# Optimization experiments

Hardware: AMD Instinct MI355X
Metric: run time of the kernel (lower is better)

The kernel has to match this reference:

```python
import jax, jax.numpy as jnp
import numpy as np

CAPACITY_FACTOR = 1.0  # fairseq Top1Gate default


def setup_inputs() -> dict:
    key = jax.random.key(0)
    ks = jax.random.split(key, 5)
    B, T, M, H, O, E = 8, 1024, 1024, 4096, 1024, 4
    return {
        "hidden_states": jax.random.normal(ks[0], (B, T, M), jnp.float32),
        "gate_w": jax.random.normal(ks[1], (M, E), jnp.float32) * 0.02,
        "fc1_w": jax.random.normal(ks[2], (E, M, H), jnp.float32) * 0.02,
        "fc1_b": jnp.zeros((E, H), jnp.float32),
        "fc2_w": jax.random.normal(ks[3], (E, H, O), jnp.float32) * 0.02,
        "fc2_b": jnp.zeros((E, O), jnp.float32),
    }


def reference(hidden_states, gate_w, fc1_w, fc1_b, fc2_w, fc2_b):
    B, T, M = hidden_states.shape
    E = gate_w.shape[1]
    S = B * T
    C = int(CAPACITY_FACTOR * -(-S // E))  # ceil(S/E)

    features = hidden_states.reshape(S, M)  # [S, M]

    # ---- Top1 gate (fairseq top1gating, eval path: no shuffle/noise) ----
    logits = features @ gate_w                      # [S, E]
    gates = jax.nn.softmax(logits, axis=1)          # [S, E]
    idx = jnp.argmax(gates, axis=1)                 # [S]
    mask1 = jax.nn.one_hot(idx, E, dtype=gates.dtype)  # [S, E]

    # load-balancing aux loss (computed before capacity dropping)
    me = jnp.mean(gates, axis=0)
    ce = jnp.mean(mask1, axis=0)
    l_aux = jnp.sum(me * ce) * E

    # capacity: position within each expert's queue; drop overflow tokens
    locations = jnp.cumsum(mask1, axis=0) - 1.0     # [S, E]
    mask1 = mask1 * (locations < C)
    loc_s = jnp.sum(locations * mask1, axis=1).astype(jnp.int32)  # [S]
    gates1_s = jnp.sum(gates * mask1, axis=1)       # [S] gate value (0 if dropped)

    # combine_weights [S, E, C] and boolean dispatch mask (as float for mm)
    combine = (gates1_s[:, None, None] * mask1[:, :, None]
               * jax.nn.one_hot(loc_s, C, dtype=gates.dtype)[:, None, :])
    dispatch = (combine > 0).astype(features.dtype)  # [S, E, C]

    # ---- dispatch via dense one-hot matmul: [E*C, S] @ [S, M] ----
    dispatch_ecs = jnp.transpose(dispatch, (1, 2, 0)).reshape(E * C, S)
    dispatched = (dispatch_ecs @ features).reshape(E, C, M)

    # ---- per-expert MLP (grouped GEMM) ----
    h = jax.nn.gelu(jnp.einsum('ecm,emh->ech', dispatched, fc1_w) + fc1_b[:, None, :])
    expert_out = jnp.einsum('ech,eho->eco', h, fc2_w) + fc2_b[:, None, :]  # [E, C, O]

    # ---- combine via dense matmul: [S, E*C] @ [E*C, O] ----
    O = expert_out.shape[-1]
    combined = combine.reshape(S, E * C) @ expert_out.reshape(E * C, O)

    return combined.reshape(B, T, O), l_aux
```

## Files before the change

kernel.cpp:

```cpp
#include <hip/hip_runtime.h>
#include <stdint.h>

#define S_TOK 8192
#define MDIM  1024
#define HDIM  4096
#define ODIM  1024
#define NEXP  4
#define CAP   2048

typedef __attribute__((ext_vector_type(8))) short short8;
typedef __attribute__((ext_vector_type(4))) float floatx4;

__device__ __forceinline__ unsigned short f2bf(float x) {
  union { float f; unsigned u; } v; v.f = x;
  unsigned r = v.u + 0x7FFFu + ((v.u >> 16) & 1u);
  return (unsigned short)(r >> 16);
}

__device__ __forceinline__ void gl_lds16(const void* g, void* l) {
  __builtin_amdgcn_global_load_lds(
      (const __attribute__((address_space(1))) void*)g,
      (__attribute__((address_space(3))) void*)l, 16, 0, 0);
}

__device__ __forceinline__ float gelu_tanh(float x) {
  float p = x * x;
  float t = x * (1.5957691216f + 0.0713548353f * p);
  float E = __expf(-t);
  return __fdividef(x, 1.0f + E);
}

__device__ __forceinline__ const char* stage_src(const char* base, int linoff,
                                                 int rowstride) {
  int row  = linoff >> 6;
  int slot = (linoff >> 4) & 3;
  int c16  = slot ^ ((row >> 1) & 3);
  return base + (size_t)row * rowstride + (c16 << 4);
}

__global__ __launch_bounds__(256) void gate_kernel(
    const float* __restrict__ feat, const float* __restrict__ gw,
    int* __restrict__ idx, float* __restrict__ gval, float* __restrict__ gsum)
{
  int wave = threadIdx.x >> 6, lane = threadIdx.x & 63;
  int s = blockIdx.x * 4 + wave;
  const float* f = feat + (size_t)s * MDIM;
  double a0 = 0, a1 = 0, a2 = 0, a3 = 0;
  #pragma unroll
  for (int j = 0; j < 16; ++j) {
    int m = lane + j * 64;
    float x = f[m];
    float4 w = ((const float4*)gw)[m];
    a0 += (double)x * w.x; a1 += (double)x * w.y;
    a2 += (double)x * w.z; a3 += (double)x * w.w;
  }
  #pragma unroll
  for (int off = 32; off; off >>= 1) {
    a0 += __shfl_down(a0, off); a1 += __shfl_down(a1, off);
    a2 += __shfl_down(a2, off); a3 += __shfl_down(a3, off);
  }
  __shared__ float bs[4];
  if (threadIdx.x < 4) bs[threadIdx.x] = 0.f;
  __syncthreads();
  if (lane == 0) {
    double lg[4] = {a0, a1, a2, a3};
    double mx = lg[0]; int bi = 0;
    #pragma unroll
    for (int e = 1; e < 4; ++e) if (lg[e] > mx) { mx = lg[e]; bi = e; }
    float ex[4]; float den = 0.f;
    #pragma unroll
    for (int e = 0; e < 4; ++e) { ex[e] = __expf((float)(lg[e] - mx)); den += ex[e]; }
    float inv = 1.f / den;
    idx[s]  = bi;
    gval[s] = ex[bi] * inv;
    #pragma unroll
    for (int e = 0; e < 4; ++e) atomicAdd(&bs[e], ex[e] * inv);
  }
  __syncthreads();
  if (threadIdx.x < 4) atomicAdd(&gsum[threadIdx.x], bs[threadIdx.x]);
}

__global__ __launch_bounds__(1024) void scan_kernel(
    const int* __restrict__ idx, int* __restrict__ perm,
    int* __restrict__ ne, const float* __restrict__ gsum,
    float* __restrict__ laux)
{
  const int tid = threadIdx.x, wave = tid >> 6, lane = tid & 63;
  __shared__ int cnt[16][4];
  __shared__ int off[16][4];
  __shared__ int tot[4];
  unsigned long long below = (lane == 0) ? 0ull : ((~0ull) >> (64 - lane));

  int myE[8], loc[8];
  int c[4] = {0, 0, 0, 0};
  #pragma unroll
  for (int j = 0; j < 8; ++j) {
    int s = wave * 512 + j * 64 + lane;
    int ev = idx[s];
    myE[j] = ev;
    #pragma unroll
    for (int e = 0; e < 4; ++e) {
      unsigned long long mb = __ballot(ev == e);
      if (ev == e) loc[j] = c[e] + __popcll(mb & below);
      c[e] += __popcll(mb);
    }
  }
  if (lane == 0) {
    #pragma unroll
    for (int e = 0; e < 4; ++e) cnt[wave][e] = c[e];
  }
  __syncthreads();
  if (tid < 64) {
    int w = tid >> 2, e = tid & 3;
    int o = 0;
    for (int w2 = 0; w2 < 16; ++w2) if (w2 < w) o += cnt[w2][e];
    off[w][e] = o;
    if (w == 15) tot[e] = o + cnt[15][e];
  }
  __syncthreads();
  #pragma unroll
  for (int j = 0; j < 8; ++j) {
    int s = wave * 512 + j * 64 + lane;
    int e = myE[j];
    int rank = off[wave][e] + loc[j];
    if (rank < CAP) perm[e * CAP + rank] = s;
  }
  if (tid < 4) ne[tid] = tot[tid] < CAP ? tot[tid] : CAP;
  if (tid == 0) {
    float l = 0.f;
    #pragma unroll
    for (int e = 0; e < 4; ++e)
      l += (gsum[e] * (1.0f / S_TOK)) * ((float)tot[e] * (1.0f / S_TOK));
    *laux = l * (float)NEXP;
  }
}

__global__ __launch_bounds__(256) void transpose_cast(
    const float* __restrict__ in, unsigned short* __restrict__ out, int R, int Cc)
{
  __shared__ unsigned short tile[64][66];
  in  += (size_t)blockIdx.z * R * Cc;
  out += (size_t)blockIdx.z * R * Cc;
  int c0 = blockIdx.x * 64, r0 = blockIdx.y * 64;
  int tx = threadIdx.x & 15;
  int ty = threadIdx.x >> 4;
  #pragma unroll
  for (int p = 0; p < 4; ++p) {
    int r = ty + p * 16;
    float4 v = *(const float4*)(in + (size_t)(r0 + r) * Cc + c0 + tx * 4);
    tile[r][tx * 4 + 0] = f2bf(v.x);
    tile[r][tx * 4 + 1] = f2bf(v.y);
    tile[r][tx * 4 + 2] = f2bf(v.z);
    tile[r][tx * 4 + 3] = f2bf(v.w);
  }
  __syncthreads();
  #pragma unroll
  for (int p = 0; p < 4; ++p) {
    int c = ty + p * 16;
    ushort4 o;
    o.x = tile[tx * 4 + 0][c];
    o.y = tile[tx * 4 + 1][c];
    o.z = tile[tx * 4 + 2][c];
    o.w = tile[tx * 4 + 3][c];
    *(ushort4*)(out + (size_t)(c0 + c) * R + r0 + tx * 4) = o;
  }
}

__global__ __launch_bounds__(256) void gather_kernel(
    const float* __restrict__ feat, const int* __restrict__ perm,
    const int* __restrict__ ne, unsigned short* __restrict__ disp)
{
  int b = blockIdx.x;
  int e = b >> 11, c = b & (CAP - 1);
  int m = threadIdx.x * 4;
  ushort4 o;
  if (c < ne[e]) {
    int s = perm[b];
    float4 v = *(const float4*)(feat + (size_t)s * MDIM + m);
    o.x = f2bf(v.x); o.y = f2bf(v.y); o.z = f2bf(v.z); o.w = f2bf(v.w);
  } else {
    o.x = o.y = o.z = o.w = 0;
  }
  *(ushort4*)(disp + (size_t)b * MDIM + m) = o;
}

__global__ __launch_bounds__(256) void fc1_kernel(
    const unsigned short* __restrict__ A, const unsigned short* __restrict__ Bt,
    const float* __restrict__ b1, unsigned short* __restrict__ Hb)
{
  const int nb = blockIdx.x, mb = blockIdx.y, e = blockIdx.z;
  const int tid = threadIdx.x, wave = tid >> 6, lane = tid & 63;

  __shared__ __align__(16) unsigned short smA[3 * 128 * 32];
  __shared__ __align__(16) unsigned short smB[3 * 128 * 32];

  const char* Ag = (const char*)(A + ((size_t)e * CAP + (size_t)mb * 128) * MDIM);
  const char* Bg = (const char*)(Bt + ((size_t)e * HDIM + (size_t)nb * 128) * MDIM);

  const int boff0 = (wave * 2 + 0) * 1024 + lane * 16;
  const int boff1 = (wave * 2 + 1) * 1024 + lane * 16;
  const char* agp0 = stage_src(Ag, boff0, 2048);
  const char* agp1 = stage_src(Ag, boff1, 2048);
  const char* bgp0 = stage_src(Bg, boff0, 2048);
  const char* bgp1 = stage_src(Bg, boff1, 2048);
  const int ldsw0 = (wave * 2 + 0) * 512;
  const int ldsw1 = (wave * 2 + 1) * 512;

  const int wm = (wave & 1) * 64, wn = (wave >> 1) * 64;
  const int fr = lane & 15, fq = lane >> 4;
  const int sqA = ((fq ^ ((wm + fr) >> 1)) & 3) * 8;
  const int sqB = ((fq ^ ((wn + fr) >> 1)) & 3) * 8;

  floatx4 acc[4][4] = {};

  const int NT = MDIM / 32;
  int c0 = 0, c1 = 1, c2 = 2;

  gl_lds16(agp0 + 0,  smA + 0 * 4096 + ldsw0);
  gl_lds16(agp1 + 0,  smA + 0 * 4096 + ldsw1);
  gl_lds16(bgp0 + 0,  smB + 0 * 4096 + ldsw0);
  gl_lds16(bgp1 + 0,  smB + 0 * 4096 + ldsw1);
  gl_lds16(agp0 + 64, smA + 1 * 4096 + ldsw0);
  gl_lds16(agp1 + 64, smA + 1 * 4096 + ldsw1);
  gl_lds16(bgp0 + 64, smB + 1 * 4096 + ldsw0);
  gl_lds16(bgp1 + 64, smB + 1 * 4096 + ldsw1);
  asm volatile("s_waitcnt vmcnt(4)" ::: "memory");
  __builtin_amdgcn_s_barrier();

  for (int kt = 0; kt < NT; ++kt) {
    if (kt + 2 < NT) {
      int kb = (kt + 2) * 64;
      gl_lds16(agp0 + kb, smA + c2 * 4096 + ldsw0);
      gl_lds16(agp1 + kb, smA + c2 * 4096 + ldsw1);
      gl_lds16(bgp0 + kb, smB + c2 * 4096 + ldsw0);
      gl_lds16(bgp1 + kb, smB + c2 * 4096 + ldsw1);
    }
    const unsigned short* sA = smA + c0 * 4096;
    const unsigned short* sB = smB + c0 * 4096;
    short8 af[4], bfr[4];
    #pragma unroll
    for (int i = 0; i < 4; ++i)
      af[i] = *(const short8*)&sA[(wm + i * 16 + fr) * 32 + sqA];
    #pragma unroll
    for (int j = 0; j < 4; ++j)
      bfr[j] = *(const short8*)&sB[(wn + j * 16 + fr) * 32 + sqB];
    #pragma unroll
    for (int i = 0; i < 4; ++i)
      #pragma unroll
      for (int j = 0; j < 4; ++j)
        acc[i][j] = __builtin_amdgcn_mfma_f32_16x16x32_bf16(bfr[j], af[i], acc[i][j], 0, 0, 0);
    if (kt + 1 < NT) {
      if (kt + 2 < NT) asm volatile("s_waitcnt vmcnt(4)" ::: "memory");
      else             asm volatile("s_waitcnt vmcnt(0)" ::: "memory");
      __builtin_amdgcn_s_barrier();
    }
    int t = c0; c0 = c1; c1 = c2; c2 = t;
  }

  unsigned short* Hrow = Hb + (size_t)e * CAP * HDIM;
  #pragma unroll
  for (int j = 0; j < 4; ++j) {
    int gn0 = nb * 128 + wn + j * 16 + fq * 4;
    float4 bv = *(const float4*)&b1[e * HDIM + gn0];
    #pragma unroll
    for (int i = 0; i < 4; ++i) {
      int m = mb * 128 + wm + i * 16 + fr;
      ushort4 o;
      o.x = f2bf(gelu_tanh(acc[i][j][0] + bv.x));
      o.y = f2bf(gelu_tanh(acc[i][j][1] + bv.y));
      o.z = f2bf(gelu_tanh(acc[i][j][2] + bv.z));
      o.w = f2bf(gelu_tanh(acc[i][j][3] + bv.w));
      *(ushort4*)&Hrow[(size_t)m * HDIM + gn0] = o;
    }
  }
}

__global__ __launch_bounds__(256) void fc2_kernel(
    const unsigned short* __restrict__ A, const unsigned short* __restrict__ Bt,
    const float* __restrict__ b2, const int* __restrict__ perm,
    const int* __restrict__ ne, const float* __restrict__ gval,
    float* __restrict__ out)
{
  const int b = blockIdx.x;
  const int wg = (b & 7) * 128 + (b >> 3);
  const int nb = wg & 7, mb = (wg >> 3) & 31, e = wg >> 8;
  const int tid = threadIdx.x, wave = tid >> 6, lane = tid & 63;

  __shared__ __align__(16) unsigned short smA[3 * 64 * 32];
  __shared__ __align__(16) unsigned short smB[3 * 128 * 32];

  const char* Ag = (const char*)(A + ((size_t)e * CAP + (size_t)mb * 64) * HDIM);
  const char* Bg = (const char*)(Bt + ((size_t)e * ODIM + (size_t)nb * 128) * HDIM);

  const char* agp = stage_src(Ag, tid * 16, 8192);
  const int boff0 = (wave * 2 + 0) * 1024 + lane * 16;
  const int boff1 = (wave * 2 + 1) * 1024 + lane * 16;
  const char* bgp0 = stage_src(Bg, boff0, 8192);
  const char* bgp1 = stage_src(Bg, boff1, 8192);

  const int ldsA_w = wave * 512;
  const int ldsB_w0 = (wave * 2 + 0) * 512;
  const int ldsB_w1 = (wave * 2 + 1) * 512;

  const int wm = (wave & 1) * 32, wn = (wave >> 1) * 64;
  const int fr = lane & 15, fq = lane >> 4;
  const int sqA = ((fq ^ ((wm + fr) >> 1)) & 3) * 8;
  const int sqB = ((fq ^ ((wn + fr) >> 1)) & 3) * 8;

  floatx4 acc[2][4] = {};

  const int NT = HDIM / 32;
  int c0 = 0, c1 = 1, c2 = 2;

  gl_lds16(agp + 0 * 64,  smA + 0 * 2048 + ldsA_w);
  gl_lds16(bgp0 + 0 * 64, smB + 0 * 4096 + ldsB_w0);
  gl_lds16(bgp1 + 0 * 64, smB + 0 * 4096 + ldsB_w1);
  gl_lds16(agp + 1 * 64,  smA + 1 * 2048 + ldsA_w);
  gl_lds16(bgp0 + 1 * 64, smB + 1 * 4096 + ldsB_w0);
  gl_lds16(bgp1 + 1 * 64, smB + 1 * 4096 + ldsB_w1);
  asm volatile("s_waitcnt vmcnt(3)" ::: "memory");
  __builtin_amdgcn_s_barrier();

  for (int kt = 0; kt < NT; ++kt) {
    if (kt + 2 < NT) {
      int kb = (kt + 2) * 64;
      gl_lds16(agp + kb,  smA + c2 * 2048 + ldsA_w);
      gl_lds16(bgp0 + kb, smB + c2 * 4096 + ldsB_w0);
      gl_lds16(bgp1 + kb, smB + c2 * 4096 + ldsB_w1);
    }
    const unsigned short* sA = smA + c0 * 2048;
    const unsigned short* sB = smB + c0 * 4096;
    short8 af[2], bfr[4];
    #pragma unroll
    for (int i = 0; i < 2; ++i)
      af[i] = *(const short8*)&sA[(wm + i * 16 + fr) * 32 + sqA];
    #pragma unroll
    for (int j = 0; j < 4; ++j)
      bfr[j] = *(const short8*)&sB[(wn + j * 16 + fr) * 32 + sqB];
    #pragma unroll
    for (int i = 0; i < 2; ++i)
      #pragma unroll
      for (int j = 0; j < 4; ++j)
        acc[i][j] = __builtin_amdgcn_mfma_f32_16x16x32_bf16(bfr[j], af[i], acc[i][j], 0, 0, 0);
    if (kt + 1 < NT) {
      if (kt + 2 < NT) asm volatile("s_waitcnt vmcnt(3)" ::: "memory");
      else             asm volatile("s_waitcnt vmcnt(0)" ::: "memory");
      __builtin_amdgcn_s_barrier();
    }
    int t = c0; c0 = c1; c1 = c2; c2 = t;
  }

  const int nE = ne[e];
  float4 b2v[4];
  #pragma unroll
  for (int j = 0; j < 4; ++j)
    b2v[j] = *(const float4*)&b2[e * ODIM + nb * 128 + wn + j * 16 + fq * 4];
  #pragma unroll
  for (int i = 0; i < 2; ++i) {
    int c = mb * 64 + wm + i * 16 + fr;
    if (c < nE) {
      int s = perm[e * CAP + c];
      float g = gval[s];
      float* orow = out + (size_t)s * ODIM + nb * 128 + wn + fq * 4;
      #pragma unroll
      for (int j = 0; j < 4; ++j) {
        float4 o;
        o.x = (acc[i][j][0] + b2v[j].x) * g;
        o.y = (acc[i][j][1] + b2v[j].y) * g;
        o.z = (acc[i][j][2] + b2v[j].z) * g;
        o.w = (acc[i][j][3] + b2v[j].w) * g;
        *(float4*)&orow[j * 16] = o;
      }
    }
  }
}

extern "C" void kernel_launch(void* const* d_in, const int* in_sizes, int n_in,
                              void* d_out, int out_size, void* d_ws, size_t ws_size,
                              hipStream_t stream) {
  const float* feat = (const float*)d_in[0];
  const float* gw   = (const float*)d_in[1];
  const float* w1   = (const float*)d_in[2];
  const float* b1   = (const float*)d_in[3];
  const float* w2   = (const float*)d_in[4];
  const float* b2   = (const float*)d_in[5];
  float* out = (float*)d_out;

  char* ws = (char*)d_ws;
  unsigned short* wt   = (unsigned short*)(ws);
  unsigned short* hbuf = (unsigned short*)(ws + 33554432);
  unsigned short* disp = (unsigned short*)(ws + 100663296);
  int*   idx  = (int*)  (ws + 117440512);
  float* gval = (float*)(ws + 117473280);
  int*   perm = (int*)  (ws + 117506048);
  float* gsum = (float*)(ws + 117538816);
  int*   ne   = (int*)  (ws + 117538832);

  hipMemsetAsync(d_out, 0, (size_t)S_TOK * ODIM * sizeof(float), stream);
  hipMemsetAsync(ws + 117538816, 0, 32, stream);

  gate_kernel<<<S_TOK / 4, 256, 0, stream>>>(feat, gw, idx, gval, gsum);
  scan_kernel<<<1, 1024, 0, stream>>>(idx, perm, ne, gsum, out + (size_t)S_TOK * ODIM);
  transpose_cast<<<dim3(HDIM / 64, MDIM / 64, NEXP), 256, 0, stream>>>(w1, wt, MDIM, HDIM);
  gather_kernel<<<NEXP * CAP, 256, 0, stream>>>(feat, perm, ne, disp);
  fc1_kernel<<<dim3(HDIM / 128, CAP / 128, NEXP), 256, 0, stream>>>(disp, wt, b1, hbuf);
  transpose_cast<<<dim3(ODIM / 64, HDIM / 64, NEXP), 256, 0, stream>>>(w2, wt, HDIM, ODIM);
  fc2_kernel<<<1024, 256, 0, stream>>>(hbuf, wt, b2, perm, ne, gval, out);
}
```

Baseline: 435.2 us.

## Remap GEMM blocks per XCD for L2 locality and enlarge fc2 tile

Block indices in fc1 and fc2 are remapped so that each XCD works on one expert and one half of the M dimension, with nearby blocks sharing A/B panels through the XCD-local L2. fc2 goes from a 64x128 tile to a 128x128 tile, so each wave holds a 4x4 accumulator set. This gives more MFMA work per LDS load and halves the grid to 512 blocks. The gate kernel now reads features as float4. The risks are higher register and LDS use in fc2, which can lower occupancy, and fewer blocks for the GPU's CUs to share.

```diff
diff --git a/kernel.cpp b/kernel.cpp
--- a/kernel.cpp
+++ b/kernel.cpp
@@ -44,15 +44,19 @@
 {
   int wave = threadIdx.x >> 6, lane = threadIdx.x & 63;
   int s = blockIdx.x * 4 + wave;
-  const float* f = feat + (size_t)s * MDIM;
+  const float4* f4 = (const float4*)(feat + (size_t)s * MDIM);
   double a0 = 0, a1 = 0, a2 = 0, a3 = 0;
   #pragma unroll
-  for (int j = 0; j < 16; ++j) {
-    int m = lane + j * 64;
-    float x = f[m];
-    float4 w = ((const float4*)gw)[m];
-    a0 += (double)x * w.x; a1 += (double)x * w.y;
-    a2 += (double)x * w.z; a3 += (double)x * w.w;
+  for (int j = 0; j < 4; ++j) {
+    int m4 = lane + j * 64;
+    float4 x = f4[m4];
+    #pragma unroll
+    for (int c = 0; c < 4; ++c) {
+      float xv = (c == 0) ? x.x : (c == 1) ? x.y : (c == 2) ? x.z : x.w;
+      float4 w = ((const float4*)gw)[m4 * 4 + c];
+      a0 += (double)xv * w.x; a1 += (double)xv * w.y;
+      a2 += (double)xv * w.z; a3 += (double)xv * w.w;
+    }
   }
   #pragma unroll
   for (int off = 32; off; off >>= 1) {
@@ -188,7 +192,12 @@
     const unsigned short* __restrict__ A, const unsigned short* __restrict__ Bt,
     const float* __restrict__ b1, unsigned short* __restrict__ Hb)
 {
-  const int nb = blockIdx.x, mb = blockIdx.y, e = blockIdx.z;
+  const int b = blockIdx.x;
+  const int xcd = b & 7, r = b >> 3;
+  const int e = xcd >> 1;
+  const int nbg = r >> 5, mbo = (r >> 2) & 7, nbl = r & 3;
+  const int nb = nbg * 4 + nbl;
+  const int mb = (xcd & 1) * 8 + mbo;
   const int tid = threadIdx.x, wave = tid >> 6, lane = tid & 63;
 
   __shared__ __align__(16) unsigned short smA[3 * 128 * 32];
@@ -282,68 +291,72 @@
     float* __restrict__ out)
 {
   const int b = blockIdx.x;
-  const int wg = (b & 7) * 128 + (b >> 3);
-  const int nb = wg & 7, mb = (wg >> 3) & 31, e = wg >> 8;
+  const int xcd = b & 7, r = b >> 3;
+  const int e = xcd >> 1;
+  const int mbg = r >> 5, nb = (r >> 2) & 7, mbl = r & 3;
+  const int mb = (xcd & 1) * 8 + mbg * 4 + mbl;
   const int tid = threadIdx.x, wave = tid >> 6, lane = tid & 63;
 
-  __shared__ __align__(16) unsigned short smA[3 * 64 * 32];
+  __shared__ __align__(16) unsigned short smA[3 * 128 * 32];
   __shared__ __align__(16) unsigned short smB[3 * 128 * 32];
 
-  const char* Ag = (const char*)(A + ((size_t)e * CAP + (size_t)mb * 64) * HDIM);
+  const char* Ag = (const char*)(A + ((size_t)e * CAP + (size_t)mb * 128) * HDIM);
   const char* Bg = (const char*)(Bt + ((size_t)e * ODIM + (size_t)nb * 128) * HDIM);
 
-  const char* agp = stage_src(Ag, tid * 16, 8192);
   const int boff0 = (wave * 2 + 0) * 1024 + lane * 16;
   const int boff1 = (wave * 2 + 1) * 1024 + lane * 16;
+  const char* agp0 = stage_src(Ag, boff0, 8192);
+  const char* agp1 = stage_src(Ag, boff1, 8192);
   const char* bgp0 = stage_src(Bg, boff0, 8192);
   const char* bgp1 = stage_src(Bg, boff1, 8192);
-
-  const int ldsA_w = wave * 512;
-  const int ldsB_w0 = (wave * 2 + 0) * 512;
-  const int ldsB_w1 = (wave * 2 + 1) * 512;
-
-  const int wm = (wave & 1) * 32, wn = (wave >> 1) * 64;
+  const int ldsw0 = (wave * 2 + 0) * 512;
+  const int ldsw1 = (wave * 2 + 1) * 512;
+
+  const int wm = (wave & 1) * 64, wn = (wave >> 1) * 64;
   const int fr = lane & 15, fq = lane >> 4;
   const int sqA = ((fq ^ ((wm + fr) >> 1)) & 3) * 8;
   const int sqB = ((fq ^ ((wn + fr) >> 1)) & 3) * 8;
 
-  floatx4 acc[2][4] = {};
+  floatx4 acc[4][4] = {};
 
   const int NT = HDIM / 32;
   int c0 = 0, c1 = 1, c2 = 2;
 
-  gl_lds16(agp + 0 * 64,  smA + 0 * 2048 + ldsA_w);
-  gl_lds16(bgp0 + 0 * 64, smB + 0 * 4096 + ldsB_w0);
-  gl_lds16(bgp1 + 0 * 64, smB + 0 * 4096 + ldsB_w1);
-  gl_lds16(agp + 1 * 64,  smA + 1 * 2048 + ldsA_w);
-  gl_lds16(bgp0 + 1 * 64, smB + 1 * 4096 + ldsB_w0);
-  gl_lds16(bgp1 + 1 * 64, smB + 1 * 4096 + ldsB_w1);
-  asm volatile("s_waitcnt vmcnt(3)" ::: "memory");
+  gl_lds16(agp0 + 0,  smA + 0 * 4096 + ldsw0);
+  gl_lds16(agp1 + 0,  smA + 0 * 4096 + ldsw1);
+  gl_lds16(bgp0 + 0,  smB + 0 * 4096 + ldsw0);
+  gl_lds16(bgp1 + 0,  smB + 0 * 4096 + ldsw1);
+  gl_lds16(agp0 + 64, smA + 1 * 4096 + ldsw0);
+  gl_lds16(agp1 + 64, smA + 1 * 4096 + ldsw1);
+  gl_lds16(bgp0 + 64, smB + 1 * 4096 + ldsw0);
+  gl_lds16(bgp1 + 64, smB + 1 * 4096 + ldsw1);
+  asm volatile("s_waitcnt vmcnt(4)" ::: "memory");
   __builtin_amdgcn_s_barrier();
 
   for (int kt = 0; kt < NT; ++kt) {
     if (kt + 2 < NT) {
       int kb = (kt + 2) * 64;
-      gl_lds16(agp + kb,  smA + c2 * 2048 + ldsA_w);
-      gl_lds16(bgp0 + kb, smB + c2 * 4096 + ldsB_w0);
-      gl_lds16(bgp1 + kb, smB + c2 * 4096 + ldsB_w1);
-    }
-    const unsigned short* sA = smA + c0 * 2048;
+      gl_lds16(agp0 + kb, smA + c2 * 4096 + ldsw0);
+      gl_lds16(agp1 + kb, smA + c2 * 4096 + ldsw1);
+      gl_lds16(bgp0 + kb, smB + c2 * 4096 + ldsw0);
+      gl_lds16(bgp1 + kb, smB + c2 * 4096 + ldsw1);
+    }
+    const unsigned short* sA = smA + c0 * 4096;
     const unsigned short* sB = smB + c0 * 4096;
-    short8 af[2], bfr[4];
-    #pragma unroll
-    for (int i = 0; i < 2; ++i)
+    short8 af[4], bfr[4];
+    #pragma unroll
+    for (int i = 0; i < 4; ++i)
       af[i] = *(const short8*)&sA[(wm + i * 16 + fr) * 32 + sqA];
     #pragma unroll
     for (int j = 0; j < 4; ++j)
       bfr[j] = *(const short8*)&sB[(wn + j * 16 + fr) * 32 + sqB];
     #pragma unroll
-    for (int i = 0; i < 2; ++i)
+    for (int i = 0; i < 4; ++i)
       #pragma unroll
       for (int j = 0; j < 4; ++j)
         acc[i][j] = __builtin_amdgcn_mfma_f32_16x16x32_bf16(bfr[j], af[i], acc[i][j], 0, 0, 0);
     if (kt + 1 < NT) {
-      if (kt + 2 < NT) asm volatile("s_waitcnt vmcnt(3)" ::: "memory");
+      if (kt + 2 < NT) asm volatile("s_waitcnt vmcnt(4)" ::: "memory");
       else             asm volatile("s_waitcnt vmcnt(0)" ::: "memory");
       __builtin_amdgcn_s_barrier();
     }
@@ -356,8 +369,8 @@
   for (int j = 0; j < 4; ++j)
     b2v[j] = *(const float4*)&b2[e * ODIM + nb * 128 + wn + j * 16 + fq * 4];
   #pragma unroll
-  for (int i = 0; i < 2; ++i) {
-    int c = mb * 64 + wm + i * 16 + fr;
+  for (int i = 0; i < 4; ++i) {
+    int c = mb * 128 + wm + i * 16 + fr;
     if (c < nE) {
       int s = perm[e * CAP + c];
       float g = gval[s];
@@ -403,7 +416,7 @@
   scan_kernel<<<1, 1024, 0, stream>>>(idx, perm, ne, gsum, out + (size_t)S_TOK * ODIM);
   transpose_cast<<<dim3(HDIM / 64, MDIM / 64, NEXP), 256, 0, stream>>>(w1, wt, MDIM, HDIM);
   gather_kernel<<<NEXP * CAP, 256, 0, stream>>>(feat, perm, ne, disp);
-  fc1_kernel<<<dim3(HDIM / 128, CAP / 128, NEXP), 256, 0, stream>>>(disp, wt, b1, hbuf);
+  fc1_kernel<<<2048, 256, 0, stream>>>(disp, wt, b1, hbuf);
   transpose_cast<<<dim3(ODIM / 64, HDIM / 64, NEXP), 256, 0, stream>>>(w2, wt, HDIM, ODIM);
-  fc2_kernel<<<1024, 256, 0, stream>>>(hbuf, wt, b2, perm, ne, gval, out);
-}
+  fc2_kernel<<<512, 256, 0, stream>>>(hbuf, wt, b2, perm, ne, gval, out);
+}
```

Result: no change. 441.7 us (+1.5%).

## Fuse gate, fc1 weight transpose and output zeroing into one prep kernel

Applied to the files above, without the earlier changes.

Merges the gating kernel, the fc1 weight transpose-cast and the output memset into one launch whose blocks branch on block index. Independent work can then overlap inside a single grid, and two launches plus the serial gaps between them go away. The gate loop now reads features as float4. It also raises wave priority around the MFMA blocks in the fc1 and fc2 GEMMs, which may change scheduling between waves. The cost is a larger, branchy kernel whose LDS tile is allocated even for gate blocks, which may lower occupancy.

```diff
diff --git a/kernel.cpp b/kernel.cpp
--- a/kernel.cpp
+++ b/kernel.cpp
@@ -38,46 +38,91 @@
   return base + (size_t)row * rowstride + (c16 << 4);
 }
 
-__global__ __launch_bounds__(256) void gate_kernel(
+__global__ __launch_bounds__(256) void prep_kernel(
     const float* __restrict__ feat, const float* __restrict__ gw,
-    int* __restrict__ idx, float* __restrict__ gval, float* __restrict__ gsum)
-{
-  int wave = threadIdx.x >> 6, lane = threadIdx.x & 63;
-  int s = blockIdx.x * 4 + wave;
-  const float* f = feat + (size_t)s * MDIM;
-  double a0 = 0, a1 = 0, a2 = 0, a3 = 0;
-  #pragma unroll
-  for (int j = 0; j < 16; ++j) {
-    int m = lane + j * 64;
-    float x = f[m];
-    float4 w = ((const float4*)gw)[m];
-    a0 += (double)x * w.x; a1 += (double)x * w.y;
-    a2 += (double)x * w.z; a3 += (double)x * w.w;
-  }
-  #pragma unroll
-  for (int off = 32; off; off >>= 1) {
-    a0 += __shfl_down(a0, off); a1 += __shfl_down(a1, off);
-    a2 += __shfl_down(a2, off); a3 += __shfl_down(a3, off);
-  }
+    const float* __restrict__ w1,
+    int* __restrict__ idx, float* __restrict__ gval, float* __restrict__ gsum,
+    unsigned short* __restrict__ wt, float* __restrict__ outz)
+{
   __shared__ float bs[4];
-  if (threadIdx.x < 4) bs[threadIdx.x] = 0.f;
-  __syncthreads();
-  if (lane == 0) {
-    double lg[4] = {a0, a1, a2, a3};
-    double mx = lg[0]; int bi = 0;
-    #pragma unroll
-    for (int e = 1; e < 4; ++e) if (lg[e] > mx) { mx = lg[e]; bi = e; }
-    float ex[4]; float den = 0.f;
-    #pragma unroll
-    for (int e = 0; e < 4; ++e) { ex[e] = __expf((float)(lg[e] - mx)); den += ex[e]; }
-    float inv = 1.f / den;
-    idx[s]  = bi;
-    gval[s] = ex[bi] * inv;
-    #pragma unroll
-    for (int e = 0; e < 4; ++e) atomicAdd(&bs[e], ex[e] * inv);
-  }
-  __syncthreads();
-  if (threadIdx.x < 4) atomicAdd(&gsum[threadIdx.x], bs[threadIdx.x]);
+  __shared__ unsigned short tile[64][66];
+  const int bid = blockIdx.x;
+
+  if (bid < 2048) {
+    int wave = threadIdx.x >> 6, lane = threadIdx.x & 63;
+    int s = bid * 4 + wave;
+    const float4* f4 = (const float4*)(feat + (size_t)s * MDIM);
+    double a0 = 0, a1 = 0, a2 = 0, a3 = 0;
+    #pragma unroll
+    for (int j = 0; j < 4; ++j) {
+      int m4 = lane + j * 64;
+      float4 x = f4[m4];
+      #pragma unroll
+      for (int c = 0; c < 4; ++c) {
+        float xv = (c == 0) ? x.x : (c == 1) ? x.y : (c == 2) ? x.z : x.w;
+        float4 w = ((const float4*)gw)[m4 * 4 + c];
+        a0 += (double)xv * w.x; a1 += (double)xv * w.y;
+        a2 += (double)xv * w.z; a3 += (double)xv * w.w;
+      }
+    }
+    #pragma unroll
+    for (int off = 32; off; off >>= 1) {
+      a0 += __shfl_down(a0, off); a1 += __shfl_down(a1, off);
+      a2 += __shfl_down(a2, off); a3 += __shfl_down(a3, off);
+    }
+    if (threadIdx.x < 4) bs[threadIdx.x] = 0.f;
+    __syncthreads();
+    if (lane == 0) {
+      double lg[4] = {a0, a1, a2, a3};
+      double mx = lg[0]; int bi = 0;
+      #pragma unroll
+      for (int e = 1; e < 4; ++e) if (lg[e] > mx) { mx = lg[e]; bi = e; }
+      float ex[4]; float den = 0.f;
+      #pragma unroll
+      for (int e = 0; e < 4; ++e) { ex[e] = __expf((float)(lg[e] - mx)); den += ex[e]; }
+      float inv = 1.f / den;
+      idx[s]  = bi;
+      gval[s] = ex[bi] * inv;
+      #pragma unroll
+      for (int e = 0; e < 4; ++e) atomicAdd(&bs[e], ex[e] * inv);
+    }
+    __syncthreads();
+    if (threadIdx.x < 4) atomicAdd(&gsum[threadIdx.x], bs[threadIdx.x]);
+  } else if (bid < 2048 + 4096) {
+    int t = bid - 2048;
+    int bz = t >> 10, rem = t & 1023;
+    int bx = rem & 63, by = rem >> 6;
+    const float* in = w1 + (size_t)bz * MDIM * HDIM;
+    unsigned short* out = wt + (size_t)bz * MDIM * HDIM;
+    int c0 = bx * 64, r0 = by * 64;
+    int tx = threadIdx.x & 15, ty = threadIdx.x >> 4;
+    #pragma unroll
+    for (int p = 0; p < 4; ++p) {
+      int r = ty + p * 16;
+      float4 v = *(const float4*)(in + (size_t)(r0 + r) * HDIM + c0 + tx * 4);
+      tile[r][tx * 4 + 0] = f2bf(v.x);
+      tile[r][tx * 4 + 1] = f2bf(v.y);
+      tile[r][tx * 4 + 2] = f2bf(v.z);
+      tile[r][tx * 4 + 3] = f2bf(v.w);
+    }
+    __syncthreads();
+    #pragma unroll
+    for (int p = 0; p < 4; ++p) {
+      int c = ty + p * 16;
+      ushort4 o;
+      o.x = tile[tx * 4 + 0][c];
+      o.y = tile[tx * 4 + 1][c];
+      o.z = tile[tx * 4 + 2][c];
+      o.w = tile[tx * 4 + 3][c];
+      *(ushort4*)(out + (size_t)(c0 + c) * MDIM + r0 + tx * 4) = o;
+    }
+  } else {
+    int t = bid - (2048 + 4096);
+    float4* p = (float4*)(outz + (size_t)t * 4096) + threadIdx.x;
+    float4 z = {0.f, 0.f, 0.f, 0.f};
+    #pragma unroll
+    for (int q = 0; q < 4; ++q) p[q * 256] = z;
+  }
 }
 
 __global__ __launch_bounds__(1024) void scan_kernel(
@@ -244,11 +289,13 @@
     #pragma unroll
     for (int j = 0; j < 4; ++j)
       bfr[j] = *(const short8*)&sB[(wn + j * 16 + fr) * 32 + sqB];
+    __builtin_amdgcn_s_setprio(1);
     #pragma unroll
     for (int i = 0; i < 4; ++i)
       #pragma unroll
       for (int j = 0; j < 4; ++j)
         acc[i][j] = __builtin_amdgcn_mfma_f32_16x16x32_bf16(bfr[j], af[i], acc[i][j], 0, 0, 0);
+    __builtin_amdgcn_s_setprio(0);
     if (kt + 1 < NT) {
       if (kt + 2 < NT) asm volatile("s_waitcnt vmcnt(4)" ::: "memory");
       else             asm volatile("s_waitcnt vmcnt(0)" ::: "memory");
@@ -337,11 +384,13 @@
     #pragma unroll
     for (int j = 0; j < 4; ++j)
       bfr[j] = *(const short8*)&sB[(wn + j * 16 + fr) * 32 + sqB];
+    __builtin_amdgcn_s_setprio(1);
     #pragma unroll
     for (int i = 0; i < 2; ++i)
       #pragma unroll
       for (int j = 0; j < 4; ++j)
         acc[i][j] = __builtin_amdgcn_mfma_f32_16x16x32_bf16(bfr[j], af[i], acc[i][j], 0, 0, 0);
+    __builtin_amdgcn_s_setprio(0);
     if (kt + 1 < NT) {
       if (kt + 2 < NT) asm volatile("s_waitcnt vmcnt(3)" ::: "memory");
       else             asm volatile("s_waitcnt vmcnt(0)" ::: "memory");
@@ -396,12 +445,11 @@
   float* gsum = (float*)(ws + 117538816);
   int*   ne   = (int*)  (ws + 117538832);
 
-  hipMemsetAsync(d_out, 0, (size_t)S_TOK * ODIM * sizeof(float), stream);
   hipMemsetAsync(ws + 117538816, 0, 32, stream);
 
-  gate_kernel<<<S_TOK / 4, 256, 0, stream>>>(feat, gw, idx, gval, gsum);
+  prep_kernel<<<2048 + 4096 + 2048, 256, 0, stream>>>(
+      feat, gw, w1, idx, gval, gsum, wt, out);
   scan_kernel<<<1, 1024, 0, stream>>>(idx, perm, ne, gsum, out + (size_t)S_TOK * ODIM);
-  transpose_cast<<<dim3(HDIM / 64, MDIM / 64, NEXP), 256, 0, stream>>>(w1, wt, MDIM, HDIM);
   gather_kernel<<<NEXP * CAP, 256, 0, stream>>>(feat, perm, ne, disp);
   fc1_kernel<<<dim3(HDIM / 128, CAP / 128, NEXP), 256, 0, stream>>>(disp, wt, b1, hbuf);
   transpose_cast<<<dim3(ODIM / 64, HDIM / 64, NEXP), 256, 0, stream>>>(w2, wt, HDIM, ODIM);
```

Result: faster. 419.3 us (-3.6%).
